# Kernel tuning notes

Measured on AMD Instinct MI355X. Metric: run time of the kernel, lower is better.

Reference implementation:

```python
import jax, jax.numpy as jnp
import numpy as np

NUM_CLASSES = 16
P = 0.8      # mitigation exponent
Q = 2.0      # compensation exponent
EPS = 0.01   # divisor smoothing
IGNORE_INDEX = 0


def setup_inputs() -> dict:
    key = jax.random.key(0)
    k1, k2 = jax.random.split(key)
    cls_score = jax.random.normal(k1, (8, NUM_CLASSES, 512, 512), dtype=jnp.float32)
    labels = jax.random.randint(k2, (8, 512, 512), 0, NUM_CLASSES, dtype=jnp.int32)
    cum_samples = jnp.zeros((NUM_CLASSES,), dtype=jnp.float32)  # persistent buffer, starts at zero
    return {"cls_score": cls_score, "labels": labels, "cum_samples": cum_samples}


def reference(cls_score, labels, cum_samples):
    C = cls_score.shape[1]
    labels = labels.reshape(-1)                                   # [M]
    logits = jnp.transpose(cls_score, (0, 2, 3, 1)).reshape(-1, C)  # [M, C]

    # buffer update: single scatter-add replaces the per-unique-label python loop
    cum = cum_samples.at[labels].add(1.0)                          # [C]
    cum_c = jnp.clip(cum, 1.0, None)

    # mitigation factor: ratio matrix over classes, gathered per pixel label
    ratio = cum_c[None, :] / cum_c[:, None]                        # [C, C]
    mit = jnp.where(ratio < 1.0, ratio ** P, 1.0)                  # [C, C]
    mitigation = mit[labels]                                       # [M, C]

    # compensation factor: detached softmax scores vs self-score
    scores = jax.nn.softmax(jax.lax.stop_gradient(logits), axis=1)  # [M, C]
    self_s = jnp.take_along_axis(scores, labels[:, None], axis=1)   # [M, 1]
    score_mat = scores / jnp.clip(self_s, EPS, None)                # [M, C]
    compensation = jnp.where(score_mat > 1.0, score_mat ** Q, 1.0)  # [M, C]

    seesaw_w = mitigation * compensation                            # [M, C]
    onehot = jax.nn.one_hot(labels, C, dtype=logits.dtype)          # [M, C]
    adj_logits = logits + jnp.log(seesaw_w) * (1.0 - onehot)        # [M, C]

    # CrossEntropyLoss(ignore_index=IGNORE_INDEX, reduction='mean')
    logp = jax.nn.log_softmax(adj_logits, axis=1)
    nll = -jnp.take_along_axis(logp, labels[:, None], axis=1)[:, 0]  # [M]
    mask = (labels != IGNORE_INDEX).astype(logits.dtype)
    loss = jnp.sum(nll * mask) / jnp.sum(mask)
    return loss
```

## Files before the change

kernel.cpp:

```cpp
#include <hip/hip_runtime.h>


constexpr int   kC      = 16;
constexpr int   kHW     = 512 * 512;
constexpr float kP      = 0.8f;
constexpr float kLogEps = -4.605170185988091f;
constexpr int   kNAcc   = 64;

__global__ __launch_bounds__(256) void init_ws_k(unsigned int* ws) {
    for (int i = threadIdx.x; i < 256 + kNAcc * 16; i += 256) ws[i] = 0u;
}

__global__ __launch_bounds__(256) void hist_k(const int4* __restrict__ lab4,
                                              unsigned int* __restrict__ histp) {
    int base = blockIdx.x * 2048 + threadIdx.x;
    int4 v[8];
    #pragma unroll
    for (int j = 0; j < 8; ++j) v[j] = lab4[base + j * 256];
    int cnt[16];
    #pragma unroll
    for (int c = 0; c < 16; ++c) cnt[c] = 0;
    #pragma unroll
    for (int j = 0; j < 8; ++j) {
        #pragma unroll
        for (int c = 0; c < 16; ++c)
            cnt[c] += (v[j].x == c) + (v[j].y == c) + (v[j].z == c) + (v[j].w == c);
    }
    #pragma unroll
    for (int c = 0; c < 16; ++c) {
        int x = cnt[c];
        #pragma unroll
        for (int off = 32; off > 0; off >>= 1) x += __shfl_down(x, off);
        cnt[c] = x;
    }
    __shared__ unsigned int sh[4 * 16];
    int wave = threadIdx.x >> 6, lane = threadIdx.x & 63;
    if (lane == 0) {
        #pragma unroll
        for (int c = 0; c < 16; ++c) sh[wave * 16 + c] = (unsigned)cnt[c];
    }
    __syncthreads();
    int t = threadIdx.x;
    if (t < 16)
        atomicAdd(&histp[t * 16], sh[t] + sh[16 + t] + sh[32 + t] + sh[48 + t]);
}

__global__ __launch_bounds__(256, 4) void seesaw_k(const float* __restrict__ cls,
                                                   const int*   __restrict__ labels,
                                                   const float* __restrict__ cum_in,
                                                   const unsigned int* __restrict__ histp,
                                                   float* __restrict__ ws) {
    __shared__ float s_plog[16];
    __shared__ float s_red[8];
    int t = threadIdx.x;
    if (t < 16) {
        float cc = fmaxf((float)histp[t * 16] + cum_in[t], 1.0f);
        s_plog[t] = kP * __logf(cc);
    }
    __syncthreads();

    int px = blockIdx.x * 256 + t;
    int b  = px >> 18;
    int hw = px & (kHW - 1);
    const float* pbase = cls + (long long)b * kC * kHW + hw;

    float l[16];
    #pragma unroll
    for (int c = 0; c < 16; ++c) l[c] = pbase[(long long)c * kHW];
    int lab = labels[px];

    float pl[16];
    #pragma unroll
    for (int c = 0; c < 16; ++c) pl[c] = s_plog[c];

    float m1 = l[0];
    float llab = l[0];
    #pragma unroll
    for (int c = 1; c < 16; ++c) {
        m1 = fmaxf(m1, l[c]);
        if (c == lab) llab = l[c];
    }
    float s = 0.0f;
    #pragma unroll
    for (int c = 0; c < 16; ++c) s += __expf(l[c] - m1);
    float K = fmaxf(llab, m1 + __logf(s) + kLogEps);
    float plab = s_plog[lab];

    float m2 = -3.0e38f;
    #pragma unroll
    for (int c = 0; c < 16; ++c) {
        float a = l[c] + fminf(0.0f, pl[c] - plab)
                       + fmaxf(0.0f, 2.0f * (l[c] - K));
        l[c] = a;
        m2 = fmaxf(m2, a);
    }
    float s2 = 0.0f;
    #pragma unroll
    for (int c = 0; c < 16; ++c) s2 += __expf(l[c] - m2);
    float nll = m2 + __logf(s2) - llab;

    float lsum = 0.0f, lcnt = 0.0f;
    if (lab != 0) { lsum = nll; lcnt = 1.0f; }
    #pragma unroll
    for (int off = 32; off > 0; off >>= 1) {
        lsum += __shfl_down(lsum, off);
        lcnt += __shfl_down(lcnt, off);
    }
    int wave = t >> 6, lane = t & 63;
    if (lane == 0) { s_red[wave] = lsum; s_red[4 + wave] = lcnt; }
    __syncthreads();
    if (t == 0) {
        float* pair = ws + 256 + (blockIdx.x & (kNAcc - 1)) * 16;
        atomicAdd(&pair[0], s_red[0] + s_red[1] + s_red[2] + s_red[3]);
        atomicAdd(&pair[1], s_red[4] + s_red[5] + s_red[6] + s_red[7]);
    }
}

__global__ void final_k(const float* __restrict__ ws, float* __restrict__ out) {
    int t = threadIdx.x;
    float a = (t < kNAcc) ? ws[256 + t * 16]     : 0.0f;
    float b = (t < kNAcc) ? ws[256 + t * 16 + 1] : 0.0f;
    #pragma unroll
    for (int off = 32; off > 0; off >>= 1) {
        a += __shfl_down(a, off);
        b += __shfl_down(b, off);
    }
    if (t == 0) out[0] = a / b;
}

extern "C" void kernel_launch(void* const* d_in, const int* in_sizes, int n_in,
                              void* d_out, int out_size, void* d_ws, size_t ws_size,
                              hipStream_t stream) {
    const float* cls    = (const float*)d_in[0];
    const int*   labels = (const int*)d_in[1];
    const float* cum_in = (const float*)d_in[2];
    float* out = (float*)d_out;
    unsigned int* ws = (unsigned int*)d_ws;

    int M  = in_sizes[1];
    int n4 = M / 4;

    init_ws_k<<<1, 256, 0, stream>>>(ws);
    hist_k<<<n4 / 2048, 256, 0, stream>>>((const int4*)labels, ws);
    seesaw_k<<<M / 256, 256, 0, stream>>>(cls, labels, cum_in, ws, (float*)ws);
    final_k<<<1, 64, 0, stream>>>((const float*)ws, out);
}
```

Measured before the change: 209.2 us.

## Vectorize seesaw kernel to float4 per thread and fold final reduction

The main kernel now processes four adjacent pixels per thread using float4 loads of each class plane and int4 label loads, and issues those loads before the shared-memory setup to overlap latency. The separate final reduction kernel is removed in favour of a last-block-done counter with threadfence in the main kernel. The histogram kernel's per-block work is also halved to launch more blocks. Register pressure rises with 64 live floats per thread, which may reduce occupancy.

```diff
diff --git a/kernel.cpp b/kernel.cpp
--- a/kernel.cpp
+++ b/kernel.cpp
@@ -6,22 +6,23 @@
 constexpr float kP      = 0.8f;
 constexpr float kLogEps = -4.605170185988091f;
 constexpr int   kNAcc   = 64;
+constexpr int   kCtrW   = 256 + kNAcc * 16;
 
 __global__ __launch_bounds__(256) void init_ws_k(unsigned int* ws) {
-    for (int i = threadIdx.x; i < 256 + kNAcc * 16; i += 256) ws[i] = 0u;
+    for (int i = threadIdx.x; i < kCtrW + 1; i += 256) ws[i] = 0u;
 }
 
 __global__ __launch_bounds__(256) void hist_k(const int4* __restrict__ lab4,
                                               unsigned int* __restrict__ histp) {
-    int base = blockIdx.x * 2048 + threadIdx.x;
-    int4 v[8];
+    int base = blockIdx.x * 1024 + threadIdx.x;
+    int4 v[4];
     #pragma unroll
-    for (int j = 0; j < 8; ++j) v[j] = lab4[base + j * 256];
+    for (int j = 0; j < 4; ++j) v[j] = lab4[base + j * 256];
     int cnt[16];
     #pragma unroll
     for (int c = 0; c < 16; ++c) cnt[c] = 0;
     #pragma unroll
-    for (int j = 0; j < 8; ++j) {
+    for (int j = 0; j < 4; ++j) {
         #pragma unroll
         for (int c = 0; c < 16; ++c)
             cnt[c] += (v[j].x == c) + (v[j].y == c) + (v[j].z == c) + (v[j].w == c);
@@ -45,62 +46,78 @@
         atomicAdd(&histp[t * 16], sh[t] + sh[16 + t] + sh[32 + t] + sh[48 + t]);
 }
 
+__device__ __forceinline__ float comp4(const float4& v, int p) {
+    return p == 0 ? v.x : p == 1 ? v.y : p == 2 ? v.z : v.w;
+}
+
 __global__ __launch_bounds__(256, 4) void seesaw_k(const float* __restrict__ cls,
                                                    const int*   __restrict__ labels,
                                                    const float* __restrict__ cum_in,
                                                    const unsigned int* __restrict__ histp,
-                                                   float* __restrict__ ws) {
+                                                   float* __restrict__ ws,
+                                                   float* __restrict__ out) {
     __shared__ float s_plog[16];
     __shared__ float s_red[8];
+    __shared__ int   s_last;
     int t = threadIdx.x;
+
+    int px0 = (blockIdx.x * 256 + t) << 2;
+    int b   = px0 >> 18;
+    int hw  = px0 & (kHW - 1);
+    const float4* pbase = (const float4*)(cls + (long long)b * kC * kHW + hw);
+    float4 v[16];
+    #pragma unroll
+    for (int c = 0; c < 16; ++c) v[c] = pbase[c * (kHW / 4)];
+    int4 lab4 = ((const int4*)labels)[blockIdx.x * 256 + t];
+
     if (t < 16) {
         float cc = fmaxf((float)histp[t * 16] + cum_in[t], 1.0f);
         s_plog[t] = kP * __logf(cc);
     }
     __syncthreads();
 
-    int px = blockIdx.x * 256 + t;
-    int b  = px >> 18;
-    int hw = px & (kHW - 1);
-    const float* pbase = cls + (long long)b * kC * kHW + hw;
-
-    float l[16];
-    #pragma unroll
-    for (int c = 0; c < 16; ++c) l[c] = pbase[(long long)c * kHW];
-    int lab = labels[px];
-
     float pl[16];
     #pragma unroll
-    for (int c = 0; c < 16; ++c) pl[c] = s_plog[c];
-
-    float m1 = l[0];
-    float llab = l[0];
-    #pragma unroll
-    for (int c = 1; c < 16; ++c) {
-        m1 = fmaxf(m1, l[c]);
-        if (c == lab) llab = l[c];
-    }
-    float s = 0.0f;
-    #pragma unroll
-    for (int c = 0; c < 16; ++c) s += __expf(l[c] - m1);
-    float K = fmaxf(llab, m1 + __logf(s) + kLogEps);
-    float plab = s_plog[lab];
-
-    float m2 = -3.0e38f;
-    #pragma unroll
-    for (int c = 0; c < 16; ++c) {
-        float a = l[c] + fminf(0.0f, pl[c] - plab)
-                       + fmaxf(0.0f, 2.0f * (l[c] - K));
-        l[c] = a;
-        m2 = fmaxf(m2, a);
-    }
-    float s2 = 0.0f;
-    #pragma unroll
-    for (int c = 0; c < 16; ++c) s2 += __expf(l[c] - m2);
-    float nll = m2 + __logf(s2) - llab;
+    for (int c = 0; c < 16; ++c)
+        pl[c] = __int_as_float(__builtin_amdgcn_readfirstlane(__float_as_int(s_plog[c])));
 
     float lsum = 0.0f, lcnt = 0.0f;
-    if (lab != 0) { lsum = nll; lcnt = 1.0f; }
+    #pragma unroll
+    for (int p = 0; p < 4; ++p) {
+        int lab = (p == 0) ? lab4.x : (p == 1) ? lab4.y : (p == 2) ? lab4.z : lab4.w;
+        float l[16];
+        #pragma unroll
+        for (int c = 0; c < 16; ++c) l[c] = comp4(v[c], p);
+
+        float m1 = l[0];
+        float llab = l[0];
+        #pragma unroll
+        for (int c = 1; c < 16; ++c) {
+            m1 = fmaxf(m1, l[c]);
+            if (c == lab) llab = l[c];
+        }
+        float s = 0.0f;
+        #pragma unroll
+        for (int c = 0; c < 16; ++c) s += __expf(l[c] - m1);
+        float K    = fmaxf(llab, m1 + __logf(s) + kLogEps);
+        float plab = s_plog[lab];
+
+        float m2 = -3.0e38f;
+        #pragma unroll
+        for (int c = 0; c < 16; ++c) {
+            float a = l[c] + fminf(0.0f, pl[c] - plab)
+                           + fmaxf(0.0f, 2.0f * (l[c] - K));
+            l[c] = a;
+            m2 = fmaxf(m2, a);
+        }
+        float s2 = 0.0f;
+        #pragma unroll
+        for (int c = 0; c < 16; ++c) s2 += __expf(l[c] - m2);
+        float nll = m2 + __logf(s2) - llab;
+
+        if (lab != 0) { lsum += nll; lcnt += 1.0f; }
+    }
+
     #pragma unroll
     for (int off = 32; off > 0; off >>= 1) {
         lsum += __shfl_down(lsum, off);
@@ -113,19 +130,24 @@
         float* pair = ws + 256 + (blockIdx.x & (kNAcc - 1)) * 16;
         atomicAdd(&pair[0], s_red[0] + s_red[1] + s_red[2] + s_red[3]);
         atomicAdd(&pair[1], s_red[4] + s_red[5] + s_red[6] + s_red[7]);
+        __threadfence();
+        unsigned done = atomicAdd((unsigned int*)ws + kCtrW, 1u);
+        s_last = (done == gridDim.x - 1) ? 1 : 0;
     }
-}
-
-__global__ void final_k(const float* __restrict__ ws, float* __restrict__ out) {
-    int t = threadIdx.x;
-    float a = (t < kNAcc) ? ws[256 + t * 16]     : 0.0f;
-    float b = (t < kNAcc) ? ws[256 + t * 16 + 1] : 0.0f;
-    #pragma unroll
-    for (int off = 32; off > 0; off >>= 1) {
-        a += __shfl_down(a, off);
-        b += __shfl_down(b, off);
+    __syncthreads();
+    if (s_last && t < 64) {
+        __threadfence();
+        float a  = __hip_atomic_load(ws + 256 + t * 16,
+                                     __ATOMIC_RELAXED, __HIP_MEMORY_SCOPE_AGENT);
+        float bb = __hip_atomic_load(ws + 256 + t * 16 + 1,
+                                     __ATOMIC_RELAXED, __HIP_MEMORY_SCOPE_AGENT);
+        #pragma unroll
+        for (int off = 32; off > 0; off >>= 1) {
+            a  += __shfl_down(a, off);
+            bb += __shfl_down(bb, off);
+        }
+        if (t == 0) out[0] = a / bb;
     }
-    if (t == 0) out[0] = a / b;
 }
 
 extern "C" void kernel_launch(void* const* d_in, const int* in_sizes, int n_in,
@@ -141,7 +163,6 @@
     int n4 = M / 4;
 
     init_ws_k<<<1, 256, 0, stream>>>(ws);
-    hist_k<<<n4 / 2048, 256, 0, stream>>>((const int4*)labels, ws);
-    seesaw_k<<<M / 256, 256, 0, stream>>>(cls, labels, cum_in, ws, (float*)ws);
-    final_k<<<1, 64, 0, stream>>>((const float*)ws, out);
+    hist_k<<<n4 / 1024, 256, 0, stream>>>((const int4*)labels, ws);
+    seesaw_k<<<M / 1024, 256, 0, stream>>>(cls, labels, cum_in, ws, (float*)ws, out);
 }
```

Result: slower. 306.5 us (+46.5%).

## Fold final reduction and plog computation into last-block epilogues, dropping a launch

Applied to the files above, without the earlier changes.

Removes the separate final reduction kernel by having the last-finishing seesaw block, detected with an atomic counter, reduce the partial sums and write the loss. The per-class log factors are now computed once by the last histogram block instead of by every seesaw block, which removes a __syncthreads and a shared-memory stage from the main kernel. The histogram grid is also doubled, with each block handling half as many labels. These changes add atomic counters and threadfences in exchange for one fewer launch and less per-block prologue work.

```diff
diff --git a/kernel.cpp b/kernel.cpp
--- a/kernel.cpp
+++ b/kernel.cpp
@@ -1,27 +1,31 @@
 #include <hip/hip_runtime.h>
 
 
-constexpr int   kC      = 16;
-constexpr int   kHW     = 512 * 512;
-constexpr float kP      = 0.8f;
-constexpr float kLogEps = -4.605170185988091f;
-constexpr int   kNAcc   = 64;
+constexpr int   kC       = 16;
+constexpr int   kHW      = 512 * 512;
+constexpr float kP       = 0.8f;
+constexpr float kLogEps  = -4.605170185988091f;
+constexpr int   kNAcc    = 64;
+constexpr int   kCtrSee  = 256 + kNAcc * 16;
+constexpr int   kCtrHist = kCtrSee + 1;
+constexpr int   kPlogW   = 1344;
 
 __global__ __launch_bounds__(256) void init_ws_k(unsigned int* ws) {
-    for (int i = threadIdx.x; i < 256 + kNAcc * 16; i += 256) ws[i] = 0u;
+    for (int i = threadIdx.x; i < kPlogW + 16; i += 256) ws[i] = 0u;
 }
 
 __global__ __launch_bounds__(256) void hist_k(const int4* __restrict__ lab4,
-                                              unsigned int* __restrict__ histp) {
-    int base = blockIdx.x * 2048 + threadIdx.x;
-    int4 v[8];
+                                              const float* __restrict__ cum_in,
+                                              unsigned int* __restrict__ ws) {
+    int base = blockIdx.x * 1024 + threadIdx.x;
+    int4 v[4];
     #pragma unroll
-    for (int j = 0; j < 8; ++j) v[j] = lab4[base + j * 256];
+    for (int j = 0; j < 4; ++j) v[j] = lab4[base + j * 256];
     int cnt[16];
     #pragma unroll
     for (int c = 0; c < 16; ++c) cnt[c] = 0;
     #pragma unroll
-    for (int j = 0; j < 8; ++j) {
+    for (int j = 0; j < 4; ++j) {
         #pragma unroll
         for (int c = 0; c < 16; ++c)
             cnt[c] += (v[j].x == c) + (v[j].y == c) + (v[j].z == c) + (v[j].w == c);
@@ -34,6 +38,7 @@
         cnt[c] = x;
     }
     __shared__ unsigned int sh[4 * 16];
+    __shared__ int s_last;
     int wave = threadIdx.x >> 6, lane = threadIdx.x & 63;
     if (lane == 0) {
         #pragma unroll
@@ -42,23 +47,31 @@
     __syncthreads();
     int t = threadIdx.x;
     if (t < 16)
-        atomicAdd(&histp[t * 16], sh[t] + sh[16 + t] + sh[32 + t] + sh[48 + t]);
+        atomicAdd(&ws[t * 16], sh[t] + sh[16 + t] + sh[32 + t] + sh[48 + t]);
+    __syncthreads();
+    if (t == 0) {
+        __threadfence();
+        unsigned d = atomicAdd(ws + kCtrHist, 1u);
+        s_last = (d == gridDim.x - 1) ? 1 : 0;
+    }
+    __syncthreads();
+    if (s_last && t < 16) {
+        __threadfence();
+        unsigned h = __hip_atomic_load(ws + t * 16,
+                                       __ATOMIC_RELAXED, __HIP_MEMORY_SCOPE_AGENT);
+        float cc = fmaxf((float)h + cum_in[t], 1.0f);
+        ((float*)ws)[kPlogW + t] = kP * __logf(cc);
+    }
 }
 
 __global__ __launch_bounds__(256, 4) void seesaw_k(const float* __restrict__ cls,
                                                    const int*   __restrict__ labels,
-                                                   const float* __restrict__ cum_in,
-                                                   const unsigned int* __restrict__ histp,
-                                                   float* __restrict__ ws) {
-    __shared__ float s_plog[16];
+                                                   const float* __restrict__ plogp,
+                                                   unsigned int* __restrict__ ws,
+                                                   float* __restrict__ out) {
     __shared__ float s_red[8];
-    int t = threadIdx.x;
-    if (t < 16) {
-        float cc = fmaxf((float)histp[t * 16] + cum_in[t], 1.0f);
-        s_plog[t] = kP * __logf(cc);
-    }
-    __syncthreads();
-
+    __shared__ int   s_last;
+    int t  = threadIdx.x;
     int px = blockIdx.x * 256 + t;
     int b  = px >> 18;
     int hw = px & (kHW - 1);
@@ -68,23 +81,22 @@
     #pragma unroll
     for (int c = 0; c < 16; ++c) l[c] = pbase[(long long)c * kHW];
     int lab = labels[px];
-
     float pl[16];
     #pragma unroll
-    for (int c = 0; c < 16; ++c) pl[c] = s_plog[c];
+    for (int c = 0; c < 16; ++c) pl[c] = plogp[c];
 
-    float m1 = l[0];
+    float m1   = l[0];
     float llab = l[0];
+    float plab = pl[0];
     #pragma unroll
     for (int c = 1; c < 16; ++c) {
         m1 = fmaxf(m1, l[c]);
-        if (c == lab) llab = l[c];
+        if (c == lab) { llab = l[c]; plab = pl[c]; }
     }
     float s = 0.0f;
     #pragma unroll
     for (int c = 0; c < 16; ++c) s += __expf(l[c] - m1);
     float K = fmaxf(llab, m1 + __logf(s) + kLogEps);
-    float plab = s_plog[lab];
 
     float m2 = -3.0e38f;
     #pragma unroll
@@ -110,22 +122,27 @@
     if (lane == 0) { s_red[wave] = lsum; s_red[4 + wave] = lcnt; }
     __syncthreads();
     if (t == 0) {
-        float* pair = ws + 256 + (blockIdx.x & (kNAcc - 1)) * 16;
+        float* pair = (float*)ws + 256 + (blockIdx.x & (kNAcc - 1)) * 16;
         atomicAdd(&pair[0], s_red[0] + s_red[1] + s_red[2] + s_red[3]);
         atomicAdd(&pair[1], s_red[4] + s_red[5] + s_red[6] + s_red[7]);
+        __threadfence();
+        unsigned done = atomicAdd(ws + kCtrSee, 1u);
+        s_last = (done == gridDim.x - 1) ? 1 : 0;
     }
-}
-
-__global__ void final_k(const float* __restrict__ ws, float* __restrict__ out) {
-    int t = threadIdx.x;
-    float a = (t < kNAcc) ? ws[256 + t * 16]     : 0.0f;
-    float b = (t < kNAcc) ? ws[256 + t * 16 + 1] : 0.0f;
-    #pragma unroll
-    for (int off = 32; off > 0; off >>= 1) {
-        a += __shfl_down(a, off);
-        b += __shfl_down(b, off);
+    __syncthreads();
+    if (s_last && t < 64) {
+        __threadfence();
+        float a  = __hip_atomic_load((float*)ws + 256 + t * 16,
+                                     __ATOMIC_RELAXED, __HIP_MEMORY_SCOPE_AGENT);
+        float bb = __hip_atomic_load((float*)ws + 256 + t * 16 + 1,
+                                     __ATOMIC_RELAXED, __HIP_MEMORY_SCOPE_AGENT);
+        #pragma unroll
+        for (int off = 32; off > 0; off >>= 1) {
+            a  += __shfl_down(a, off);
+            bb += __shfl_down(bb, off);
+        }
+        if (t == 0) out[0] = a / bb;
     }
-    if (t == 0) out[0] = a / b;
 }
 
 extern "C" void kernel_launch(void* const* d_in, const int* in_sizes, int n_in,
@@ -141,7 +158,7 @@
     int n4 = M / 4;
 
     init_ws_k<<<1, 256, 0, stream>>>(ws);
-    hist_k<<<n4 / 2048, 256, 0, stream>>>((const int4*)labels, ws);
-    seesaw_k<<<M / 256, 256, 0, stream>>>(cls, labels, cum_in, ws, (float*)ws);
-    final_k<<<1, 64, 0, stream>>>((const float*)ws, out);
+    hist_k<<<n4 / 1024, 256, 0, stream>>>((const int4*)labels, cum_in, ws);
+    seesaw_k<<<M / 256, 256, 0, stream>>>(cls, labels,
+                                          (const float*)ws + kPlogW, ws, out);
 }
```

After: 528.0 us. 152% more time.
